# Kernel tuning notes

Measured on AMD Instinct MI355X. Metric: run time of the kernel, lower is better.

The kernel has to match this reference:

```python
import jax, jax.numpy as jnp
import numpy as np

MAX_REL = 64  # max_relative_position
LN_EPS = 1e-5


def _relative_positions(seq_len):
    r = jnp.arange(seq_len)
    rel = jnp.clip(r[None, :] - r[:, None], -MAX_REL, MAX_REL) + MAX_REL
    return rel  # [S, S] int32 in [0, 2*MAX_REL]


def setup_inputs() -> dict:
    key = jax.random.key(0)
    ks = jax.random.split(key, 8)
    B, S, H = 8, 1024, 128
    sd = 1.0 / np.sqrt(H)
    return {
        "x": jax.random.normal(ks[0], (B, S, H), jnp.float32),
        "Wq": jax.random.normal(ks[1], (H, H), jnp.float32) * sd,
        "bq": jnp.zeros((H,), jnp.float32),
        "Wk": jax.random.normal(ks[2], (H, H), jnp.float32) * sd,
        "bk": jnp.zeros((H,), jnp.float32),
        "Wv": jax.random.normal(ks[3], (H, H), jnp.float32) * sd,
        "bv": jnp.zeros((H,), jnp.float32),
        "rel_k": jax.random.normal(ks[4], (2 * MAX_REL + 1, H), jnp.float32),
        "rel_v": jax.random.normal(ks[5], (2 * MAX_REL + 1, H), jnp.float32),
        "Wo": jax.random.normal(ks[6], (H, H), jnp.float32) * sd,
        "bo": jnp.zeros((H,), jnp.float32),
        "gamma": jnp.ones((H,), jnp.float32),
        "beta": jnpp if False else jnp.zeros((H,), jnp.float32),
    }


def reference(x, Wq, bq, Wk, bk, Wv, bv, rel_k, rel_v, Wo, bo, gamma, beta):
    B, S, H = x.shape
    scale = jnp.sqrt(jnp.asarray(H, x.dtype))

    q = x @ Wq + bq  # [B,S,H]
    k = x @ Wk + bk
    v = x @ Wv + bv

    scores = jnp.einsum("bih,bjh->bij", q, k) / scale  # [B,S,S]

    relpos = _relative_positions(S)            # [S,S] int
    rk = rel_k[relpos]                          # [S,S,H] gather
    scores = scores + jnp.einsum("bih,ijh->bij", q, rk)

    attn = jax.nn.softmax(scores, axis=-1)      # dropout = identity (eval)

    ctx = jnp.einsum("bij,bjh->bih", attn, v)
    rv = rel_v[relpos]                          # [S,S,H] gather
    ctx = ctx + jnp.einsum("bij,ijh->bih", attn, rv)

    out = ctx @ Wo + bo

    # residual + LayerNorm
    y = out + x
    mu = jnp.mean(y, axis=-1, keepdims=True)
    var = jnp.mean(jnp.square(y - mu), axis=-1, keepdims=True)
    y = (y - mu) * jax.lax.rsqrt(var + LN_EPS) * gamma + beta
    return y, attn
```

## Files before the change

kernel.cpp:

```cpp
#include <hip/hip_runtime.h>

constexpr int Bn = 8, Sn = 1024, Hn = 128, Rn = 129, RLD = 132;
constexpr float INV_SCALE = 0.088388347648318447f;
constexpr size_t YEL = (size_t)Bn * Sn * Hn;

typedef short bf16x8 __attribute__((ext_vector_type(8)));
typedef short v4s __attribute__((ext_vector_type(4)));
typedef float f32x4 __attribute__((ext_vector_type(4)));
typedef int v4i __attribute__((ext_vector_type(4)));

__device__ __forceinline__ float bf2f(short s) {
    unsigned u = ((unsigned)(unsigned short)s) << 16;
    float f; __builtin_memcpy(&f, &u, 4); return f;
}
__device__ __forceinline__ short f2bf(float f) {
    unsigned u; __builtin_memcpy(&u, &f, 4);
    unsigned r = (u + 0x7fffu + ((u >> 16) & 1u)) >> 16;
    return (short)(r & 0xffffu);
}

__global__ __launch_bounds__(384) void build_relcat(
    const float* __restrict__ rel_k, short* __restrict__ relcat)
{
    const int p = blockIdx.x, c = threadIdx.x;
    const int j = (c < 256) ? (c & 127) : (c - 256);
    float v = rel_k[p * Hn + j];
    short h = f2bf(v);
    relcat[p * 384 + c] = (c < 256) ? h : f2bf(v - bf2f(h));
}

__global__ __launch_bounds__(256) void build_bcat(
    const float* __restrict__ rel_v, const float* __restrict__ Wo,
    short* __restrict__ BcatT)
{
    int idx = blockIdx.x * 256 + threadIdx.x;
    int k = idx >> 7, n = idx & 127;
    float v;
    if (k < 128) v = Wo[k * Hn + n];
    else if (k < 257) {
        int p = k - 128; float a = 0.f;
        for (int h = 0; h < Hn; ++h) a += rel_v[p * Hn + h] * Wo[h * Hn + n];
        v = a;
    } else v = 0.f;
    BcatT[n * 320 + k] = f2bf(v);
}

__global__ __launch_bounds__(256) void proj(
    const float* __restrict__ X,
    const float* __restrict__ Wq, const float* __restrict__ bq,
    const float* __restrict__ Wk, const float* __restrict__ bk,
    const float* __restrict__ Wv, const float* __restrict__ bv,
    short* __restrict__ qh, short* __restrict__ qcat,
    short* __restrict__ kh, short* __restrict__ vT)
{
    __shared__ float xs[64][128];
    __shared__ float wsm[32][128];
    const int tid = threadIdx.x;
    const int sel = blockIdx.y;
    const int row0 = blockIdx.x * 64;
    const float* W = (sel == 0) ? Wq : (sel == 1) ? Wk : Wv;
    const float* bias = (sel == 0) ? bq : (sel == 1) ? bk : bv;

#pragma unroll
    for (int it = 0; it < 8; ++it) {
        int u = tid + it * 256;
        int r = u >> 5, c4 = (u & 31) * 4;
        *(float4*)&xs[r][c4] = *(const float4*)(X + (size_t)(row0 + r) * 128 + c4);
    }

    const int rg = tid >> 5, cg = tid & 31;
    float acc[8][4] = {};
    for (int kc = 0; kc < 128; kc += 32) {
#pragma unroll
        for (int it = 0; it < 4; ++it) {
            int u = tid + it * 256;
            int kk = u >> 5, c4 = (u & 31) * 4;
            *(float4*)&wsm[kk][c4] = *(const float4*)(W + (size_t)(kc + kk) * 128 + c4);
        }
        __syncthreads();
#pragma unroll 8
        for (int kk = 0; kk < 32; ++kk) {
            float wv[4];
#pragma unroll
            for (int c = 0; c < 4; ++c) wv[c] = wsm[kk][cg + c * 32];
#pragma unroll
            for (int r = 0; r < 8; ++r) {
                float xv = xs[rg * 8 + r][kc + kk];
#pragma unroll
                for (int c = 0; c < 4; ++c) acc[r][c] += xv * wv[c];
            }
        }
        __syncthreads();
    }

#pragma unroll
    for (int c = 0; c < 4; ++c) {
        int col = cg + c * 32;
        float bv2 = bias[col];
#pragma unroll
        for (int r = 0; r < 8; ++r) {
            int row = row0 + rg * 8 + r;
            float v = acc[r][c] + bv2;
            short h = f2bf(v);
            if (sel == 0) {
                qh[(size_t)row * 128 + col] = h;
                qcat[(size_t)row * 256 + col] = h;
                qcat[(size_t)row * 256 + 128 + col] = f2bf(v - bf2f(h));
            } else if (sel == 1) {
                kh[(size_t)row * 128 + col] = h;
            } else {
                int b = row >> 10, i = row & (Sn - 1);
                vT[(size_t)b * 131072 + (size_t)col * 1024 + i] = h;
            }
        }
    }
}

__global__ __launch_bounds__(256) void qrel_gemm(
    const short* __restrict__ qcat, const short* __restrict__ relcat,
    float* __restrict__ qrel)
{
    __shared__ short As[64][72];
    __shared__ short Bs[64][72];
    const int tid = threadIdx.x;
    const int wave = tid >> 6, lane = tid & 63;
    const int quad = lane >> 4, l15 = lane & 15;
    const int row0 = blockIdx.x * 64, col0 = blockIdx.y * 64;

    f32x4 acc[4] = {};
    for (int kc = 0; kc < 384; kc += 64) {
#pragma unroll
        for (int it = 0; it < 2; ++it) {
            int u = tid + it * 256;
            int r = u >> 3, c8 = (u & 7) * 8;
            int srcc = kc + c8;
            if (srcc >= 256) srcc -= 256;
            *(v4i*)&As[r][c8] = *(const v4i*)(qcat + (size_t)(row0 + r) * 256 + srcc);
        }
#pragma unroll
        for (int it = 0; it < 2; ++it) {
            int u = tid + it * 256;
            int r = u >> 3, c8 = (u & 7) * 8;
            v4i val = {0, 0, 0, 0};
            if (col0 + r < Rn)
                val = *(const v4i*)(relcat + (size_t)(col0 + r) * 384 + kc + c8);
            *(v4i*)&Bs[r][c8] = val;
        }
        __syncthreads();
#pragma unroll
        for (int ks = 0; ks < 64; ks += 32) {
            bf16x8 af = *(const bf16x8*)&As[wave * 16 + l15][ks + quad * 8];
#pragma unroll
            for (int nt = 0; nt < 4; ++nt) {
                bf16x8 bf = *(const bf16x8*)&Bs[nt * 16 + l15][ks + quad * 8];
                acc[nt] = __builtin_amdgcn_mfma_f32_16x16x32_bf16(af, bf, acc[nt], 0, 0, 0);
            }
        }
        __syncthreads();
    }
    const int rloc0 = wave * 16 + quad * 4;
#pragma unroll
    for (int nt = 0; nt < 4; ++nt) {
        int col = col0 + nt * 16 + l15;
#pragma unroll
        for (int r = 0; r < 4; ++r) {
            if (col < Rn)
                qrel[(size_t)(row0 + rloc0 + r) * RLD + col] = acc[nt][r];
        }
    }
}

__global__ __launch_bounds__(512) void fused_attn(
    const short* __restrict__ qh, const short* __restrict__ kh,
    const short* __restrict__ vT, const float* __restrict__ qrel_g,
    float* __restrict__ attn_g, float* __restrict__ arel_g,
    float* __restrict__ ctx_g)
{
    __shared__ __align__(16) float smem[18560];
    float* Ssc = smem;
    float* QrL = smem + 16448;
    short* Pb  = (short*)smem;

    const int tid = threadIdx.x;
    const int w = tid >> 6, lane = tid & 63;
    const int quad = lane >> 4, l15 = lane & 15;
    const int bz = blockIdx.z;
    const int row0 = blockIdx.x * 16;
    const size_t grow0 = (size_t)bz * Sn + row0;

#pragma unroll
    for (int rr = 0; rr < 2; ++rr) {
        int r = w * 2 + rr;
        const float* src = qrel_g + (grow0 + r) * RLD;
        QrL[r * 132 + lane] = src[lane];
        QrL[r * 132 + lane + 64] = src[lane + 64];
        if (lane < 4) QrL[r * 132 + 128 + lane] = src[128 + lane];
    }

    bf16x8 afr[4];
#pragma unroll
    for (int kk = 0; kk < 4; ++kk)
        afr[kk] = *(const bf16x8*)(qh + (grow0 + l15) * 128 + kk * 32 + quad * 8);
    __syncthreads();

#pragma unroll
    for (int nt = 0; nt < 8; ++nt) {
        int colb = w * 128 + nt * 16;
        f32x4 acc = {};
#pragma unroll
        for (int kk = 0; kk < 4; ++kk) {
            bf16x8 bfr = *(const bf16x8*)(kh + ((size_t)bz * Sn + colb + l15) * 128 + kk * 32 + quad * 8);
            acc = __builtin_amdgcn_mfma_f32_16x16x32_bf16(afr[kk], bfr, acc, 0, 0, 0);
        }
        int col = colb + l15;
#pragma unroll
        for (int r = 0; r < 4; ++r) {
            int lr = quad * 4 + r;
            int i = row0 + lr;
            int d = col - i; d = (d < -64) ? -64 : (d > 64 ? 64 : d);
            Ssc[lr * 1028 + col] = acc[r] * INV_SCALE + QrL[lr * 132 + d + 64];
        }
    }
    __syncthreads();

    float av[2][16];
    float lov[2], hiv[2];
#pragma unroll
    for (int rr = 0; rr < 2; ++rr) {
        int lr = w * 2 + rr, i = row0 + lr;
        float* base = &Ssc[lr * 1028 + lane * 16];
        float4 x0 = *(float4*)(base + 0), x1 = *(float4*)(base + 4);
        float4 x2 = *(float4*)(base + 8), x3 = *(float4*)(base + 12);
        float* a = av[rr];
        a[0]=x0.x; a[1]=x0.y; a[2]=x0.z; a[3]=x0.w;
        a[4]=x1.x; a[5]=x1.y; a[6]=x1.z; a[7]=x1.w;
        a[8]=x2.x; a[9]=x2.y; a[10]=x2.z; a[11]=x2.w;
        a[12]=x3.x; a[13]=x3.y; a[14]=x3.z; a[15]=x3.w;
        float mx = a[0];
#pragma unroll
        for (int j = 1; j < 16; ++j) mx = fmaxf(mx, a[j]);
#pragma unroll
        for (int m = 1; m < 64; m <<= 1) mx = fmaxf(mx, __shfl_xor(mx, m));
        float s = 0.f;
#pragma unroll
        for (int j = 0; j < 16; ++j) { a[j] = __expf(a[j] - mx); s += a[j]; }
#pragma unroll
        for (int m = 1; m < 64; m <<= 1) s += __shfl_xor(s, m);
        float inv = 1.0f / s;
        float lo = 0.f, hi = 0.f;
#pragma unroll
        for (int j = 0; j < 16; ++j) {
            a[j] *= inv;
            int col = lane * 16 + j;
            lo += (col <= i - 64) ? a[j] : 0.f;
            hi += (col >= i + 64) ? a[j] : 0.f;
        }
#pragma unroll
        for (int m = 1; m < 64; m <<= 1) { lo += __shfl_xor(lo, m); hi += __shfl_xor(hi, m); }
        lov[rr] = lo; hiv[rr] = hi;
        float* dst = attn_g + (grow0 + lr) * Sn + lane * 16;
        *(float4*)(dst + 0)  = float4{a[0], a[1], a[2], a[3]};
        *(float4*)(dst + 4)  = float4{a[4], a[5], a[6], a[7]};
        *(float4*)(dst + 8)  = float4{a[8], a[9], a[10], a[11]};
        *(float4*)(dst + 12) = float4{a[12], a[13], a[14], a[15]};
    }
    __syncthreads();

#pragma unroll
    for (int rr = 0; rr < 2; ++rr) {
        int lr = w * 2 + rr;
        short t16[16];
#pragma unroll
        for (int j = 0; j < 16; ++j) t16[j] = f2bf(av[rr][j]);
        v4i pk0, pk1;
        __builtin_memcpy(&pk0, t16, 16);
        __builtin_memcpy(&pk1, t16 + 8, 16);
        *(v4i*)&Pb[lr * 1032 + lane * 16] = pk0;
        *(v4i*)&Pb[lr * 1032 + lane * 16 + 8] = pk1;
    }
    __syncthreads();

#pragma unroll
    for (int rr = 0; rr < 2; ++rr) {
        int lr = w * 2 + rr, i = row0 + lr;
        float* arow = arel_g + (grow0 + lr) * RLD;
        {
            float v;
            if (lane == 0) v = lov[rr];
            else { int c = i + lane - 64; v = (c >= 0 && c < Sn) ? bf2f(Pb[lr * 1032 + c]) : 0.f; }
            arow[lane] = v;
        }
        {
            int p = lane + 64;
            int c = i + p - 64;
            arow[p] = (c >= 0 && c < Sn) ? bf2f(Pb[lr * 1032 + c]) : 0.f;
        }
        if (lane < 4) {
            int p = lane + 128;
            arow[p] = (p == 128) ? hiv[rr] : 0.f;
        }
    }

    f32x4 cacc = {};
#pragma unroll 8
    for (int kk = 0; kk < 32; ++kk) {
        bf16x8 a = *(const bf16x8*)&Pb[l15 * 1032 + kk * 32 + quad * 8];
        bf16x8 b = *(const bf16x8*)(vT + (size_t)bz * 131072 + (size_t)(w * 16 + l15) * 1024 + kk * 32 + quad * 8);
        cacc = __builtin_amdgcn_mfma_f32_16x16x32_bf16(a, b, cacc, 0, 0, 0);
    }
#pragma unroll
    for (int r = 0; r < 4; ++r) {
        int lr = quad * 4 + r;
        ctx_g[(grow0 + lr) * 128 + w * 16 + l15] = cacc[r];
    }
}

__global__ __launch_bounds__(256) void ln_gemm(
    const float* __restrict__ ctx, const float* __restrict__ arel,
    const short* __restrict__ BcatT, const float* __restrict__ bo,
    const float* __restrict__ X, const float* __restrict__ gamma,
    const float* __restrict__ beta, float* __restrict__ y)
{
    __shared__ float rs1[16][4];
    __shared__ float rs2[16][4];
    const int tid = threadIdx.x;
    const int w = tid >> 6, lane = tid & 63;
    const int quad = lane >> 4, l15 = lane & 15;
    const int rows0 = blockIdx.x * 16;
    const int arow = rows0 + l15;

    f32x4 acc[2] = {};
#pragma unroll
    for (int kk = 0; kk < 9; ++kk) {
        bf16x8 a;
        if (kk < 4) {
            const float* src = ctx + (size_t)arow * 128 + kk * 32 + quad * 8;
            float4 w0 = *(const float4*)src, w1 = *(const float4*)(src + 4);
            short t[8] = { f2bf(w0.x), f2bf(w0.y), f2bf(w0.z), f2bf(w0.w),
                           f2bf(w1.x), f2bf(w1.y), f2bf(w1.z), f2bf(w1.w) };
            __builtin_memcpy(&a, t, 16);
        } else if (kk < 8) {
            const float* src = arel + (size_t)arow * RLD + (kk - 4) * 32 + quad * 8;
            float4 w0 = *(const float4*)src, w1 = *(const float4*)(src + 4);
            short t[8] = { f2bf(w0.x), f2bf(w0.y), f2bf(w0.z), f2bf(w0.w),
                           f2bf(w1.x), f2bf(w1.y), f2bf(w1.z), f2bf(w1.w) };
            __builtin_memcpy(&a, t, 16);
        } else {
            short t[8] = {0,0,0,0,0,0,0,0};
            if (quad == 0) {
                float4 w0 = *(const float4*)(arel + (size_t)arow * RLD + 128);
                t[0] = f2bf(w0.x); t[1] = f2bf(w0.y); t[2] = f2bf(w0.z); t[3] = f2bf(w0.w);
            }
            __builtin_memcpy(&a, t, 16);
        }
#pragma unroll
        for (int t2 = 0; t2 < 2; ++t2) {
            int n = (w * 2 + t2) * 16 + l15;
            bf16x8 b = *(const bf16x8*)(BcatT + (size_t)n * 320 + kk * 32 + quad * 8);
            acc[t2] = __builtin_amdgcn_mfma_f32_16x16x32_bf16(a, b, acc[t2], 0, 0, 0);
        }
    }

    float vv[2][4];
#pragma unroll
    for (int t2 = 0; t2 < 2; ++t2) {
        int col = w * 32 + t2 * 16 + l15;
        float bv = bo[col], gv;
        (void)gv;
#pragma unroll
        for (int r = 0; r < 4; ++r) {
            int grow = rows0 + quad * 4 + r;
            vv[t2][r] = acc[t2][r] + bv + X[(size_t)grow * 128 + col];
        }
    }
#pragma unroll
    for (int r = 0; r < 4; ++r) {
        float s = vv[0][r] + vv[1][r];
#pragma unroll
        for (int m = 1; m < 16; m <<= 1) s += __shfl_xor(s, m);
        if (l15 == 0) rs1[quad * 4 + r][w] = s;
    }
    __syncthreads();
    float mu[4];
#pragma unroll
    for (int r = 0; r < 4; ++r) {
        int lr = quad * 4 + r;
        mu[r] = (rs1[lr][0] + rs1[lr][1] + rs1[lr][2] + rs1[lr][3]) * (1.f / 128.f);
    }
#pragma unroll
    for (int r = 0; r < 4; ++r) {
        float d0 = vv[0][r] - mu[r], d1 = vv[1][r] - mu[r];
        float s = d0 * d0 + d1 * d1;
#pragma unroll
        for (int m = 1; m < 16; m <<= 1) s += __shfl_xor(s, m);
        if (l15 == 0) rs2[quad * 4 + r][w] = s;
    }
    __syncthreads();
#pragma unroll
    for (int r = 0; r < 4; ++r) {
        int lr = quad * 4 + r;
        int grow = rows0 + lr;
        float var = (rs2[lr][0] + rs2[lr][1] + rs2[lr][2] + rs2[lr][3]) * (1.f / 128.f);
        float inv = rsqrtf(var + 1e-5f);
#pragma unroll
        for (int t2 = 0; t2 < 2; ++t2) {
            int col = w * 32 + t2 * 16 + l15;
            y[(size_t)grow * 128 + col] = (vv[t2][r] - mu[r]) * inv * gamma[col] + beta[col];
        }
    }
}

extern "C" void kernel_launch(void* const* d_in, const int* in_sizes, int n_in,
                              void* d_out, int out_size, void* d_ws, size_t ws_size,
                              hipStream_t stream) {
    const float* x     = (const float*)d_in[0];
    const float* Wq    = (const float*)d_in[1];
    const float* bq    = (const float*)d_in[2];
    const float* Wk    = (const float*)d_in[3];
    const float* bk    = (const float*)d_in[4];
    const float* Wv    = (const float*)d_in[5];
    const float* bv    = (const float*)d_in[6];
    const float* rel_k = (const float*)d_in[7];
    const float* rel_v = (const float*)d_in[8];
    const float* Wo    = (const float*)d_in[9];
    const float* bo    = (const float*)d_in[10];
    const float* gamma = (const float*)d_in[11];
    const float* beta  = (const float*)d_in[12];

    char* ws = (char*)d_ws;
    short* qh     = (short*)(ws + 0);
    short* kh     = (short*)(ws + 2097152);
    short* vT     = (short*)(ws + 4194304);
    short* qcat   = (short*)(ws + 6291456);
    float* qrel   = (float*)(ws + 10485760);
    short* relcat = (short*)(ws + 14811136);
    short* BcatT  = (short*)relcat;
    float* ctx    = (float*)qcat;

    float* y_out = (float*)d_out;
    float* attn  = (float*)d_out + YEL;

    build_relcat<<<dim3(Rn), 384, 0, stream>>>(rel_k, relcat);
    proj<<<dim3(128, 3), 256, 0, stream>>>(x, Wq, bq, Wk, bk, Wv, bv, qh, qcat, kh, vT);
    qrel_gemm<<<dim3(128, 3), 256, 0, stream>>>(qcat, relcat, qrel);
    build_bcat<<<dim3(160), 256, 0, stream>>>(rel_v, Wo, BcatT);

    fused_attn<<<dim3(64, 1, Bn), 512, 0, stream>>>(qh, kh, vT, qrel, attn, qrel, ctx);

    ln_gemm<<<dim3(512), 256, 0, stream>>>(ctx, qrel, BcatT, bo, x, gamma, beta, y_out);
}
```

Baseline: 180.6 us.

## Keep attention scores in registers and reduce softmax across waves via shared memory

The fused attention kernel no longer stages the full 16x1024 fp32 score tile in LDS. Scores stay in MFMA accumulator registers, and row max, sum and the relative-position tail sums are reduced across the 8 waves through small shared arrays. K fragment loads are double-buffered ahead of the MFMAs, and launch bounds now request higher occupancy. The change cuts LDS footprint and traffic, which allows more resident blocks, at the cost of extra barriers and scalar (non-vectorized) global stores of the attention matrix.

```diff
diff --git a/kernel.cpp b/kernel.cpp
--- a/kernel.cpp
+++ b/kernel.cpp
@@ -170,16 +170,15 @@
     }
 }
 
-__global__ __launch_bounds__(512) void fused_attn(
+__global__ __launch_bounds__(512, 4) void fused_attn(
     const short* __restrict__ qh, const short* __restrict__ kh,
     const short* __restrict__ vT, const float* __restrict__ qrel_g,
     float* __restrict__ attn_g, float* __restrict__ arel_g,
     float* __restrict__ ctx_g)
 {
-    __shared__ __align__(16) float smem[18560];
-    float* Ssc = smem;
-    float* QrL = smem + 16448;
-    short* Pb  = (short*)smem;
+    __shared__ __align__(16) short Pb[16][1048];
+    __shared__ float QrL[16][132];
+    __shared__ float redM[16][8], redS[16][8], redL[16][8], redH[16][8];
 
     const int tid = threadIdx.x;
     const int w = tid >> 6, lane = tid & 63;
@@ -192,130 +191,136 @@
     for (int rr = 0; rr < 2; ++rr) {
         int r = w * 2 + rr;
         const float* src = qrel_g + (grow0 + r) * RLD;
-        QrL[r * 132 + lane] = src[lane];
-        QrL[r * 132 + lane + 64] = src[lane + 64];
-        if (lane < 4) QrL[r * 132 + 128 + lane] = src[128 + lane];
+        QrL[r][lane] = src[lane];
+        QrL[r][lane + 64] = src[lane + 64];
+        if (lane < 4) QrL[r][128 + lane] = src[128 + lane];
     }
 
     bf16x8 afr[4];
 #pragma unroll
     for (int kk = 0; kk < 4; ++kk)
         afr[kk] = *(const bf16x8*)(qh + (grow0 + l15) * 128 + kk * 32 + quad * 8);
-    __syncthreads();
-
+
+    const short* khb = kh + (size_t)bz * Sn * 128;
+    f32x4 acc[8] = {};
+    bf16x8 bb[2][4];
+#pragma unroll
+    for (int kk = 0; kk < 4; ++kk)
+        bb[0][kk] = *(const bf16x8*)(khb + (size_t)(w * 128 + l15) * 128 + kk * 32 + quad * 8);
 #pragma unroll
     for (int nt = 0; nt < 8; ++nt) {
-        int colb = w * 128 + nt * 16;
-        f32x4 acc = {};
-#pragma unroll
-        for (int kk = 0; kk < 4; ++kk) {
-            bf16x8 bfr = *(const bf16x8*)(kh + ((size_t)bz * Sn + colb + l15) * 128 + kk * 32 + quad * 8);
-            acc = __builtin_amdgcn_mfma_f32_16x16x32_bf16(afr[kk], bfr, acc, 0, 0, 0);
-        }
-        int col = colb + l15;
-#pragma unroll
-        for (int r = 0; r < 4; ++r) {
-            int lr = quad * 4 + r;
-            int i = row0 + lr;
+        int cur = nt & 1;
+        if (nt < 7) {
+#pragma unroll
+            for (int kk = 0; kk < 4; ++kk)
+                bb[cur ^ 1][kk] = *(const bf16x8*)(khb +
+                    (size_t)(w * 128 + (nt + 1) * 16 + l15) * 128 + kk * 32 + quad * 8);
+        }
+#pragma unroll
+        for (int kk = 0; kk < 4; ++kk)
+            acc[nt] = __builtin_amdgcn_mfma_f32_16x16x32_bf16(afr[kk], bb[cur][kk], acc[nt], 0, 0, 0);
+    }
+    __syncthreads();
+
+    float mx[4];
+#pragma unroll
+    for (int r = 0; r < 4; ++r) {
+        int lr = quad * 4 + r, i = row0 + lr;
+        float m = -3.4e38f;
+#pragma unroll
+        for (int nt = 0; nt < 8; ++nt) {
+            int col = w * 128 + nt * 16 + l15;
             int d = col - i; d = (d < -64) ? -64 : (d > 64 ? 64 : d);
-            Ssc[lr * 1028 + col] = acc[r] * INV_SCALE + QrL[lr * 132 + d + 64];
-        }
-    }
-    __syncthreads();
-
-    float av[2][16];
-    float lov[2], hiv[2];
+            float v = acc[nt][r] * INV_SCALE + QrL[lr][d + 64];
+            acc[nt][r] = v;
+            m = fmaxf(m, v);
+        }
+#pragma unroll
+        for (int msk = 1; msk < 16; msk <<= 1) m = fmaxf(m, __shfl_xor(m, msk));
+        if (l15 == 0) redM[lr][w] = m;
+    }
+    __syncthreads();
+#pragma unroll
+    for (int r = 0; r < 4; ++r) {
+        int lr = quad * 4 + r;
+        float m = redM[lr][0];
+#pragma unroll
+        for (int j = 1; j < 8; ++j) m = fmaxf(m, redM[lr][j]);
+        mx[r] = m;
+    }
+
+#pragma unroll
+    for (int r = 0; r < 4; ++r) {
+        int lr = quad * 4 + r, i = row0 + lr;
+        float s = 0.f, lo = 0.f, hi = 0.f;
+#pragma unroll
+        for (int nt = 0; nt < 8; ++nt) {
+            float e = __expf(acc[nt][r] - mx[r]);
+            acc[nt][r] = e;
+            s += e;
+            int col = w * 128 + nt * 16 + l15;
+            lo += (col <= i - 64) ? e : 0.f;
+            hi += (col >= i + 64) ? e : 0.f;
+        }
+#pragma unroll
+        for (int msk = 1; msk < 16; msk <<= 1) {
+            s += __shfl_xor(s, msk);
+            lo += __shfl_xor(lo, msk);
+            hi += __shfl_xor(hi, msk);
+        }
+        if (l15 == 0) { redS[lr][w] = s; redL[lr][w] = lo; redH[lr][w] = hi; }
+    }
+    __syncthreads();
+
+#pragma unroll
+    for (int r = 0; r < 4; ++r) {
+        int lr = quad * 4 + r;
+        float s = 0.f;
+#pragma unroll
+        for (int j = 0; j < 8; ++j) s += redS[lr][j];
+        float inv = 1.0f / s;
+        float* arow = attn_g + (grow0 + lr) * Sn;
+#pragma unroll
+        for (int nt = 0; nt < 8; ++nt) {
+            int col = w * 128 + nt * 16 + l15;
+            float v = acc[nt][r] * inv;
+            arow[col] = v;
+            Pb[lr][col] = f2bf(v);
+        }
+    }
+    __syncthreads();
+
 #pragma unroll
     for (int rr = 0; rr < 2; ++rr) {
         int lr = w * 2 + rr, i = row0 + lr;
-        float* base = &Ssc[lr * 1028 + lane * 16];
-        float4 x0 = *(float4*)(base + 0), x1 = *(float4*)(base + 4);
-        float4 x2 = *(float4*)(base + 8), x3 = *(float4*)(base + 12);
-        float* a = av[rr];
-        a[0]=x0.x; a[1]=x0.y; a[2]=x0.z; a[3]=x0.w;
-        a[4]=x1.x; a[5]=x1.y; a[6]=x1.z; a[7]=x1.w;
-        a[8]=x2.x; a[9]=x2.y; a[10]=x2.z; a[11]=x2.w;
-        a[12]=x3.x; a[13]=x3.y; a[14]=x3.z; a[15]=x3.w;
-        float mx = a[0];
-#pragma unroll
-        for (int j = 1; j < 16; ++j) mx = fmaxf(mx, a[j]);
-#pragma unroll
-        for (int m = 1; m < 64; m <<= 1) mx = fmaxf(mx, __shfl_xor(mx, m));
-        float s = 0.f;
-#pragma unroll
-        for (int j = 0; j < 16; ++j) { a[j] = __expf(a[j] - mx); s += a[j]; }
-#pragma unroll
-        for (int m = 1; m < 64; m <<= 1) s += __shfl_xor(s, m);
+        float s = 0.f, lo = 0.f, hi = 0.f;
+#pragma unroll
+        for (int j = 0; j < 8; ++j) { s += redS[lr][j]; lo += redL[lr][j]; hi += redH[lr][j]; }
         float inv = 1.0f / s;
-        float lo = 0.f, hi = 0.f;
-#pragma unroll
-        for (int j = 0; j < 16; ++j) {
-            a[j] *= inv;
-            int col = lane * 16 + j;
-            lo += (col <= i - 64) ? a[j] : 0.f;
-            hi += (col >= i + 64) ? a[j] : 0.f;
-        }
-#pragma unroll
-        for (int m = 1; m < 64; m <<= 1) { lo += __shfl_xor(lo, m); hi += __shfl_xor(hi, m); }
-        lov[rr] = lo; hiv[rr] = hi;
-        float* dst = attn_g + (grow0 + lr) * Sn + lane * 16;
-        *(float4*)(dst + 0)  = float4{a[0], a[1], a[2], a[3]};
-        *(float4*)(dst + 4)  = float4{a[4], a[5], a[6], a[7]};
-        *(float4*)(dst + 8)  = float4{a[8], a[9], a[10], a[11]};
-        *(float4*)(dst + 12) = float4{a[12], a[13], a[14], a[15]};
-    }
-    __syncthreads();
-
-#pragma unroll
-    for (int rr = 0; rr < 2; ++rr) {
-        int lr = w * 2 + rr;
-        short t16[16];
-#pragma unroll
-        for (int j = 0; j < 16; ++j) t16[j] = f2bf(av[rr][j]);
-        v4i pk0, pk1;
-        __builtin_memcpy(&pk0, t16, 16);
-        __builtin_memcpy(&pk1, t16 + 8, 16);
-        *(v4i*)&Pb[lr * 1032 + lane * 16] = pk0;
-        *(v4i*)&Pb[lr * 1032 + lane * 16 + 8] = pk1;
-    }
-    __syncthreads();
-
-#pragma unroll
-    for (int rr = 0; rr < 2; ++rr) {
-        int lr = w * 2 + rr, i = row0 + lr;
         float* arow = arel_g + (grow0 + lr) * RLD;
-        {
-            float v;
-            if (lane == 0) v = lov[rr];
-            else { int c = i + lane - 64; v = (c >= 0 && c < Sn) ? bf2f(Pb[lr * 1032 + c]) : 0.f; }
-            arow[lane] = v;
-        }
-        {
-            int p = lane + 64;
-            int c = i + p - 64;
-            arow[p] = (c >= 0 && c < Sn) ? bf2f(Pb[lr * 1032 + c]) : 0.f;
-        }
-        if (lane < 4) {
-            int p = lane + 128;
-            arow[p] = (p == 128) ? hiv[rr] : 0.f;
-        }
+        float v0;
+        if (lane == 0) v0 = lo * inv;
+        else { int c = i + lane - 64; v0 = (c >= 0 && c < Sn) ? bf2f(Pb[lr][c]) : 0.f; }
+        arow[lane] = v0;
+        int c1 = i + lane;
+        arow[lane + 64] = (c1 < Sn) ? bf2f(Pb[lr][c1]) : 0.f;
+        if (lane < 4) arow[128 + lane] = (lane == 0) ? hi * inv : 0.f;
     }
 
     f32x4 cacc = {};
+    const short* vtb = vT + (size_t)bz * 131072 + (size_t)(w * 16 + l15) * 1024;
 #pragma unroll 8
     for (int kk = 0; kk < 32; ++kk) {
-        bf16x8 a = *(const bf16x8*)&Pb[l15 * 1032 + kk * 32 + quad * 8];
-        bf16x8 b = *(const bf16x8*)(vT + (size_t)bz * 131072 + (size_t)(w * 16 + l15) * 1024 + kk * 32 + quad * 8);
+        bf16x8 a = *(const bf16x8*)&Pb[l15][kk * 32 + quad * 8];
+        bf16x8 b = *(const bf16x8*)(vtb + kk * 32 + quad * 8);
         cacc = __builtin_amdgcn_mfma_f32_16x16x32_bf16(a, b, cacc, 0, 0, 0);
     }
 #pragma unroll
-    for (int r = 0; r < 4; ++r) {
-        int lr = quad * 4 + r;
-        ctx_g[(grow0 + lr) * 128 + w * 16 + l15] = cacc[r];
-    }
-}
-
-__global__ __launch_bounds__(256) void ln_gemm(
+    for (int r = 0; r < 4; ++r)
+        ctx_g[(grow0 + quad * 4 + r) * 128 + w * 16 + l15] = cacc[r];
+}
+
+__global__ __launch_bounds__(256, 4) void ln_gemm(
     const float* __restrict__ ctx, const float* __restrict__ arel,
     const short* __restrict__ BcatT, const float* __restrict__ bo,
     const float* __restrict__ X, const float* __restrict__ gamma,
@@ -365,8 +370,7 @@
 #pragma unroll
     for (int t2 = 0; t2 < 2; ++t2) {
         int col = w * 32 + t2 * 16 + l15;
-        float bv = bo[col], gv;
-        (void)gv;
+        float bv = bo[col];
 #pragma unroll
         for (int r = 0; r < 4; ++r) {
             int grow = rows0 + quad * 4 + r;
```

Result: faster. 172.5 us (-4.5%).
